# Kernel optimization log

Measured on AMD Instinct MI355X. Metric: run time of the kernel, lower is better.

Reference implementation:

```python
import jax, jax.numpy as jnp
import numpy as np

NUM_HEADS = 16


def setup_inputs() -> dict:
    key = jax.random.key(0)
    k1, k2, k3 = jax.random.split(key, 3)
    B, L, H = 2, 2048, 1024
    return {
        "key": jax.random.normal(k1, (B, L, H), dtype=jnp.float32),
        "W_ctx": jax.random.normal(k2, (H, H), dtype=jnp.float32) * (1.0 / np.sqrt(H)),
        "b_ctx": jax.random.normal(k3, (H,), dtype=jnp.float32) * 0.01,
    }


def reference(key, W_ctx, b_ctx):
    # Note: the torch module defines q/k/v Linear layers but never calls them
    # in forward(); it reshapes the raw input into heads directly.
    B, L, H = key.shape
    dh = H // NUM_HEADS
    # [B, L, H] -> [B, nh, L, dh]
    x = key.reshape(B, L, NUM_HEADS, dh).transpose(0, 2, 1, 3)
    # QK^T then scale by sqrt(head_dim) (key.shape[-1] after head split)
    scores = jnp.einsum("bhqd,bhkd->bhqk", x, x) * (1.0 / np.float32(np.sqrt(dh)))
    attn = jax.nn.softmax(scores, axis=-1)  # dropout p treated as eval/identity
    ctx = jnp.einsum("bhqk,bhkd->bhqd", attn, x)
    # [B, nh, L, dh] -> [B, L, H]
    ctx = ctx.transpose(0, 2, 1, 3).reshape(B, L, H)
    # context_transform: nn.Linear(H, H, bias=True)
    return ctx @ W_ctx.T + b_ctx
```

## Files before the change

kernel.cpp:

```cpp
#include <hip/hip_runtime.h>
#include <stdint.h>

#define NH     16
#define LSEQ   2048
#define DH     64
#define HDIM   1024
#define BATCH  2

typedef __attribute__((ext_vector_type(8))) short bf16x8;
typedef __attribute__((ext_vector_type(8))) unsigned short u16x8;
typedef __attribute__((ext_vector_type(4))) float f32x4;
typedef __attribute__((ext_vector_type(16))) float f32x16;

static __device__ inline unsigned short f2bs(float f) {
    union { float f; uint32_t u; } v; v.f = f;
    uint32_t u = v.u;
    return (unsigned short)((u + 0x7FFFu + ((u >> 16) & 1u)) >> 16);
}

static __device__ inline unsigned int cvtpk(float lo, float hi) {
    unsigned int r;
    asm("v_cvt_pk_bf16_f32 %0, %1, %2" : "=v"(r) : "v"(lo), "v"(hi));
    return r;
}
static __device__ inline void pl32swap(unsigned int &a, unsigned int &b) {
    asm volatile("v_permlane32_swap_b32 %0, %1" : "+v"(a), "+v"(b));
}

#define GLOAD_LDS(gp, lp) \
    __builtin_amdgcn_global_load_lds((const __attribute__((address_space(1))) void*)(gp), \
                                     (__attribute__((address_space(3))) void*)(lp), 16, 0, 0)

#define MFMA32(A, B, C) __builtin_amdgcn_mfma_f32_32x32x16_bf16((A), (B), (C), 0, 0, 0)

#define QK_SCALE 0.42466083f

__global__ __launch_bounds__(256) void prep_kernel(const float* __restrict__ x,
                                                   const float* __restrict__ W,
                                                   unsigned short* __restrict__ xb,
                                                   unsigned short* __restrict__ xt,
                                                   unsigned short* __restrict__ wbt) {
    const int lt = blockIdx.x, bh = blockIdx.y;
    const int bid = bh * 32 + lt;
    const int t = threadIdx.x;

    if (t < 128) {
        const int gid = bid * 128 + t;
        const int n  = gid >> 7;
        const int kc = gid & 127;
        const float* src = W + (size_t)n * 1024 + kc * 8;
        float4 f0 = *(const float4*)(src);
        float4 f1 = *(const float4*)(src + 4);
        u16x8 v;
        v[0]=f2bs(f0.x); v[1]=f2bs(f0.y); v[2]=f2bs(f0.z); v[3]=f2bs(f0.w);
        v[4]=f2bs(f1.x); v[5]=f2bs(f1.y); v[6]=f2bs(f1.z); v[7]=f2bs(f1.w);
        const int nt = n >> 7, rn = n & 127;
        const int kt = kc >> 3, c = kc & 7;
        *(u16x8*)(wbt + (((size_t)nt * 16 + kt) * 128 + rn) * 64 + ((c ^ (rn & 7)) * 8)) = v;
    }

    const int b = bh >> 4, h = bh & 15;
    const int r = t >> 2, cp = t & 3;

    __shared__ __align__(16) unsigned short Sm[64][72];

    const float* src = x + ((size_t)(b * LSEQ + lt * 64 + r)) * HDIM + h * DH + cp * 16;
    float4 f0 = *(const float4*)(src);
    float4 f1 = *(const float4*)(src + 4);
    float4 f2 = *(const float4*)(src + 8);
    float4 f3 = *(const float4*)(src + 12);
    u16x8 lo, hi;
    lo[0]=f2bs(f0.x); lo[1]=f2bs(f0.y); lo[2]=f2bs(f0.z); lo[3]=f2bs(f0.w);
    lo[4]=f2bs(f1.x); lo[5]=f2bs(f1.y); lo[6]=f2bs(f1.z); lo[7]=f2bs(f1.w);
    hi[0]=f2bs(f2.x); hi[1]=f2bs(f2.y); hi[2]=f2bs(f2.z); hi[3]=f2bs(f2.w);
    hi[4]=f2bs(f3.x); hi[5]=f2bs(f3.y); hi[6]=f2bs(f3.z); hi[7]=f2bs(f3.w);
    u16x8 slo, shi;
    slo[0]=f2bs(f0.x*QK_SCALE); slo[1]=f2bs(f0.y*QK_SCALE); slo[2]=f2bs(f0.z*QK_SCALE); slo[3]=f2bs(f0.w*QK_SCALE);
    slo[4]=f2bs(f1.x*QK_SCALE); slo[5]=f2bs(f1.y*QK_SCALE); slo[6]=f2bs(f1.z*QK_SCALE); slo[7]=f2bs(f1.w*QK_SCALE);
    shi[0]=f2bs(f2.x*QK_SCALE); shi[1]=f2bs(f2.y*QK_SCALE); shi[2]=f2bs(f2.z*QK_SCALE); shi[3]=f2bs(f2.w*QK_SCALE);
    shi[4]=f2bs(f3.x*QK_SCALE); shi[5]=f2bs(f3.y*QK_SCALE); shi[6]=f2bs(f3.z*QK_SCALE); shi[7]=f2bs(f3.w*QK_SCALE);

    {
        unsigned short* xbase = xb + (size_t)bh * 131072
                              + ((size_t)lt * 2 + (r >> 5)) * 2048 + cp * 512 + (r & 31) * 8;
        *(u16x8*)(xbase)       = slo;
        *(u16x8*)(xbase + 256) = shi;
    }
    *(u16x8*)&Sm[r][cp * 16]     = lo;
    *(u16x8*)&Sm[r][cp * 16 + 8] = hi;
    __syncthreads();

    {
        const int d = t >> 2, part = (t & 3) * 16;
        unsigned short* vbase = xt + (size_t)bh * 131072 + (size_t)lt * 4096
                              + (d >> 5) * 2048 + (part >> 4) * 512 + (d & 31) * 8;
        u16x8 g0, g1;
        #pragma unroll
        for (int i = 0; i < 8; ++i) g0[i] = Sm[part + i][d];
        #pragma unroll
        for (int i = 0; i < 8; ++i) g1[i] = Sm[part + 8 + i][d];
        *(u16x8*)(vbase)       = g0;
        *(u16x8*)(vbase + 256) = g1;
    }
}

__global__ __launch_bounds__(256, 3) void attn_kernel(const unsigned short* __restrict__ xb,
                                                      const unsigned short* __restrict__ xt,
                                                      unsigned short* __restrict__ ctxt) {
    const int bh = blockIdx.x;
    const int qt = blockIdx.y;
    const int tid = threadIdx.x;
    const int w = tid >> 6, lane = tid & 63;
    const int l31 = lane & 31, hh = lane >> 5;

    const char* xbB = (const char*)(xb + (size_t)bh * 131072);
    const char* xtB = (const char*)(xt + (size_t)bh * 131072);

    bf16x8 qf[4];
    {
        const char* qbase = xbB + (size_t)(qt * 4 + w) * 4096 + lane * 16;
        #pragma unroll
        for (int ds = 0; ds < 4; ++ds)
            qf[ds] = *(const bf16x8*)(qbase + ds * 1024);
    }

    bf16x8 ones;
    #pragma unroll
    for (int i = 0; i < 8; ++i) ones[i] = (short)0x3F80;

    f32x16 accA, accB, accS;
    #pragma unroll
    for (int r = 0; r < 16; ++r) { accA[r] = 0.f; accB[r] = 0.f; accS[r] = 0.f; }

    const char* ka = xbB + lane * 16;
    const char* va = xtB + lane * 16;

    for (int tt = 0; tt < 32; ++tt) {
        bf16x8 kfa[4], kfb[4];
        #pragma unroll
        for (int ds = 0; ds < 4; ++ds) {
            kfa[ds] = *(const bf16x8*)(ka + ds * 1024);
            kfb[ds] = *(const bf16x8*)(ka + 4096 + ds * 1024);
        }

        f32x16 s0, s1;
        #pragma unroll
        for (int r = 0; r < 16; ++r) { s0[r] = 0.f; s1[r] = 0.f; }
        __builtin_amdgcn_s_setprio(1);
        #pragma unroll
        for (int ds = 0; ds < 4; ++ds) {
            s0 = MFMA32(kfa[ds], qf[ds], s0);
            s1 = MFMA32(kfb[ds], qf[ds], s1);
        }
        __builtin_amdgcn_s_setprio(0);

        bf16x8 vfa[4], vfb[4];
        #pragma unroll
        for (int ks = 0; ks < 4; ++ks) {
            vfa[ks] = *(const bf16x8*)(va + ks * 1024);
            vfb[ks] = *(const bf16x8*)(va + 4096 + ks * 1024);
        }
        ka += 8192;
        va += 8192;

        #pragma unroll
        for (int r = 0; r < 16; ++r) {
            s0[r] = __builtin_amdgcn_exp2f(s0[r]);
            s1[r] = __builtin_amdgcn_exp2f(s1[r]);
        }

        bf16x8 pa[4];
        #pragma unroll
        for (int ks = 0; ks < 4; ++ks) {
            const int r0 = (ks & 1) * 8;
            unsigned int x0, y0, x1, y1;
            if (ks < 2) {
                x0 = cvtpk(s0[r0 + 0], s0[r0 + 1]);
                y0 = cvtpk(s0[r0 + 4], s0[r0 + 5]);
                x1 = cvtpk(s0[r0 + 2], s0[r0 + 3]);
                y1 = cvtpk(s0[r0 + 6], s0[r0 + 7]);
            } else {
                x0 = cvtpk(s1[r0 + 0], s1[r0 + 1]);
                y0 = cvtpk(s1[r0 + 4], s1[r0 + 5]);
                x1 = cvtpk(s1[r0 + 2], s1[r0 + 3]);
                y1 = cvtpk(s1[r0 + 6], s1[r0 + 7]);
            }
            pl32swap(x0, y0);
            pl32swap(x1, y1);
            union { unsigned int u[4]; bf16x8 v; } pu;
            pu.u[0] = x0; pu.u[1] = x1; pu.u[2] = y0; pu.u[3] = y1;
            pa[ks] = pu.v;
        }

        __builtin_amdgcn_s_setprio(1);
        #pragma unroll
        for (int ks = 0; ks < 4; ++ks) {
            accA = MFMA32(pa[ks], vfa[ks], accA);
            accB = MFMA32(pa[ks], vfb[ks], accB);
            accS = MFMA32(pa[ks], ones, accS);
        }
        __builtin_amdgcn_s_setprio(0);
    }

    const int b = bh >> 4, hd = bh & 15;
    const int mt = b * 16 + qt;
    unsigned short* tbase = ctxt + ((size_t)mt * 16 + hd) * 128 * 64;
    const int c80 = l31 >> 3, c81 = 4 + (l31 >> 3), ce = l31 & 7;
    #pragma unroll
    for (int r = 0; r < 16; ++r) {
        const float iv = 1.0f / accS[r];
        const int crow = (r & 3) + 8 * (r >> 2) + 4 * hh;
        const int rr = w * 32 + crow;
        unsigned short* rowp = tbase + rr * 64;
        const int sw = rr & 7;
        rowp[((c80 ^ sw) * 8) + ce] = f2bs(accA[r] * iv);
        rowp[((c81 ^ sw) * 8) + ce] = f2bs(accB[r] * iv);
    }
}

__global__ __launch_bounds__(256) void proj_kernel(const unsigned short* __restrict__ ctxt,
                                                   const unsigned short* __restrict__ wbt,
                                                   const float* __restrict__ bias,
                                                   float* __restrict__ out) {
    const int ntb = blockIdx.x;
    const int mtb = blockIdx.y;
    const int tid = threadIdx.x;
    const int w = tid >> 6, lane = tid & 63;
    const int la = lane & 15, quad = lane >> 4;
    const int wm = (w >> 1) * 64, wn = (w & 1) * 64;

    __shared__ __align__(16) unsigned short As[3][8192];
    __shared__ __align__(16) unsigned short Bs[3][8192];

    const unsigned short* abase = ctxt + (size_t)mtb * 16 * 8192;
    const unsigned short* bbase = wbt  + (size_t)ntb * 16 * 8192;

    const int sw0 = ((quad)     ^ (la & 7)) * 8;
    const int sw1 = ((quad + 4) ^ (la & 7)) * 8;

    const f32x4 fzero = {0.f, 0.f, 0.f, 0.f};
    f32x4 acc[4][4];
    #pragma unroll
    for (int i = 0; i < 4; ++i)
        #pragma unroll
        for (int j = 0; j < 4; ++j) acc[i][j] = fzero;

    #pragma unroll
    for (int s = 0; s < 2; ++s) {
        const char* asrc = (const char*)(abase + s * 8192);
        const char* bsrc = (const char*)(bbase + s * 8192);
        #pragma unroll
        for (int j = 0; j < 4; ++j) {
            const int fc = j * 256 + tid;
            GLOAD_LDS(asrc + fc * 16, (char*)As[s] + fc * 16);
            GLOAD_LDS(bsrc + fc * 16, (char*)Bs[s] + fc * 16);
        }
    }
    asm volatile("s_waitcnt vmcnt(8)" ::: "memory");
    __builtin_amdgcn_s_barrier();

    for (int kt = 0; kt < 16; ++kt) {
        if (kt < 14) {
            const int nb = (kt + 2) % 3;
            const char* asrc = (const char*)(abase + (kt + 2) * 8192);
            const char* bsrc = (const char*)(bbase + (kt + 2) * 8192);
            #pragma unroll
            for (int j = 0; j < 4; ++j) {
                const int fc = j * 256 + tid;
                GLOAD_LDS(asrc + fc * 16, (char*)As[nb] + fc * 16);
                GLOAD_LDS(bsrc + fc * 16, (char*)Bs[nb] + fc * 16);
            }
        }

        const unsigned short* Ab = As[kt % 3];
        const unsigned short* Bb = Bs[kt % 3];
        #pragma unroll
        for (int ks2 = 0; ks2 < 2; ++ks2) {
            const int sw = ks2 ? sw1 : sw0;
            bf16x8 af[4], bfr[4];
            #pragma unroll
            for (int mt = 0; mt < 4; ++mt) af[mt]  = *(const bf16x8*)&Ab[(wm + mt * 16 + la) * 64 + sw];
            #pragma unroll
            for (int nt = 0; nt < 4; ++nt) bfr[nt] = *(const bf16x8*)&Bb[(wn + nt * 16 + la) * 64 + sw];
            #pragma unroll
            for (int mt = 0; mt < 4; ++mt)
                #pragma unroll
                for (int nt = 0; nt < 4; ++nt)
                    acc[mt][nt] = __builtin_amdgcn_mfma_f32_16x16x32_bf16(af[mt], bfr[nt], acc[mt][nt], 0, 0, 0);
        }

        if (kt < 14) {
            asm volatile("s_waitcnt vmcnt(8)" ::: "memory");
            __builtin_amdgcn_s_barrier();
        } else if (kt == 14) {
            asm volatile("s_waitcnt vmcnt(0)" ::: "memory");
            __builtin_amdgcn_s_barrier();
        }
    }

    const int m0 = mtb * 128, n0 = ntb * 128;
    #pragma unroll
    for (int nt = 0; nt < 4; ++nt) {
        const int n = n0 + wn + nt * 16 + la;
        const float bv = bias[n];
        #pragma unroll
        for (int mt = 0; mt < 4; ++mt)
            #pragma unroll
            for (int r = 0; r < 4; ++r) {
                const int m = m0 + wm + mt * 16 + quad * 4 + r;
                out[(size_t)m * HDIM + n] = acc[mt][nt][r] + bv;
            }
    }
}

extern "C" void kernel_launch(void* const* d_in, const int* in_sizes, int n_in,
                              void* d_out, int out_size, void* d_ws, size_t ws_size,
                              hipStream_t stream) {
    const float* x    = (const float*)d_in[0];
    const float* W    = (const float*)d_in[1];
    const float* bias = (const float*)d_in[2];
    float* out = (float*)d_out;

    unsigned short* ctxt = (unsigned short*)d_ws;
    unsigned short* xbp  = (unsigned short*)((char*)d_ws + ( 8u << 20));
    unsigned short* xtp  = (unsigned short*)((char*)d_ws + (16u << 20));
    unsigned short* wbt  = (unsigned short*)((char*)d_ws + (24u << 20));

    prep_kernel<<<dim3(32, 32), 256, 0, stream>>>(x, W, xbp, xtp, wbt);
    attn_kernel<<<dim3(32, 16), 256, 0, stream>>>(xbp, xtp, ctxt);
    proj_kernel<<<dim3(8, 32), 256, 0, stream>>>(ctxt, wbt, bias, out);
}
```

Baseline: 142.6 us.

## Stage K/V tiles through triple-buffered LDS with async global-to-LDS loads

Each attention block now cooperatively streams K and V tiles into a three-slot LDS ring using direct global-to-LDS loads, prefetching two tiles ahead, and all four waves read their fragments from LDS. Before, every wave loaded the same K/V tiles from global memory on its own. The aim is to cut redundant global/L2 traffic and hide load latency. In exchange it adds 48KB of LDS per block, a barrier every iteration, and lowers the occupancy hint from 3 to 2 blocks per CU.

After: 135.9 us. 1.05x faster.

```diff
diff --git a/kernel.cpp b/kernel.cpp
--- a/kernel.cpp
+++ b/kernel.cpp
@@ -104,7 +104,7 @@
     }
 }
 
-__global__ __launch_bounds__(256, 3) void attn_kernel(const unsigned short* __restrict__ xb,
+__global__ __launch_bounds__(256, 2) void attn_kernel(const unsigned short* __restrict__ xb,
                                                       const unsigned short* __restrict__ xt,
                                                       unsigned short* __restrict__ ctxt) {
     const int bh = blockIdx.x;
@@ -113,6 +113,8 @@
     const int w = tid >> 6, lane = tid & 63;
     const int l31 = lane & 31, hh = lane >> 5;
 
+    __shared__ __align__(16) char KVL[3][16384];
+
     const char* xbB = (const char*)(xb + (size_t)bh * 131072);
     const char* xtB = (const char*)(xt + (size_t)bh * 131072);
 
@@ -132,15 +134,36 @@
     #pragma unroll
     for (int r = 0; r < 16; ++r) { accA[r] = 0.f; accB[r] = 0.f; accS[r] = 0.f; }
 
-    const char* ka = xbB + lane * 16;
-    const char* va = xtB + lane * 16;
+    const int soff = tid * 16;
+
+#define STAGE(t, s) { \
+        const char* kp_ = xbB + (size_t)(t) * 8192; \
+        const char* vp_ = xtB + (size_t)(t) * 8192; \
+        GLOAD_LDS(kp_ + soff,        KVL[s] + soff); \
+        GLOAD_LDS(kp_ + 4096 + soff, KVL[s] + 4096 + soff); \
+        GLOAD_LDS(vp_ + soff,        KVL[s] + 8192 + soff); \
+        GLOAD_LDS(vp_ + 4096 + soff, KVL[s] + 12288 + soff); \
+    }
+
+    STAGE(0, 0);
+    STAGE(1, 1);
+    asm volatile("s_waitcnt vmcnt(4)" ::: "memory");
+    __builtin_amdgcn_s_barrier();
 
     for (int tt = 0; tt < 32; ++tt) {
+        if (tt < 30) {
+            const int nb = (tt + 2) % 3;
+            STAGE(tt + 2, nb);
+        }
+
+        const char* kb = KVL[tt % 3] + lane * 16;
+        const char* vb = KVL[tt % 3] + 8192 + lane * 16;
+
         bf16x8 kfa[4], kfb[4];
         #pragma unroll
         for (int ds = 0; ds < 4; ++ds) {
-            kfa[ds] = *(const bf16x8*)(ka + ds * 1024);
-            kfb[ds] = *(const bf16x8*)(ka + 4096 + ds * 1024);
+            kfa[ds] = *(const bf16x8*)(kb + ds * 1024);
+            kfb[ds] = *(const bf16x8*)(kb + 4096 + ds * 1024);
         }
 
         f32x16 s0, s1;
@@ -157,11 +180,9 @@
         bf16x8 vfa[4], vfb[4];
         #pragma unroll
         for (int ks = 0; ks < 4; ++ks) {
-            vfa[ks] = *(const bf16x8*)(va + ks * 1024);
-            vfb[ks] = *(const bf16x8*)(va + 4096 + ks * 1024);
-        }
-        ka += 8192;
-        va += 8192;
+            vfa[ks] = *(const bf16x8*)(vb + ks * 1024);
+            vfb[ks] = *(const bf16x8*)(vb + 4096 + ks * 1024);
+        }
 
         #pragma unroll
         for (int r = 0; r < 16; ++r) {
@@ -200,7 +221,15 @@
             accS = MFMA32(pa[ks], ones, accS);
         }
         __builtin_amdgcn_s_setprio(0);
-    }
+
+        if (tt < 30) {
+            asm volatile("s_waitcnt vmcnt(4)" ::: "memory");
+        } else {
+            asm volatile("s_waitcnt vmcnt(0)" ::: "memory");
+        }
+        __builtin_amdgcn_s_barrier();
+    }
+#undef STAGE
 
     const int b = bh >> 4, hd = bh & 15;
     const int mt = b * 16 + qt;
```
